# Performance work log

Measured on AMD Instinct MI355X. Metric: run time of the kernel, lower is better.

## Reference

```python
import jax, jax.numpy as jnp
import numpy as np

D_K = 64
SCALE = jnp.sqrt(jnp.float32(D_K))

def setup_inputs() -> dict:
    key = jax.random.key(0)
    kq, kk, kv = jax.random.split(key, 3)
    shape = (2, 16, 2048, D_K)  # [batch, heads, seq, d_k]
    return {
        "Q": jax.random.normal(kq, shape, dtype=jnp.float32),
        "K": jax.random.normal(kk, shape, dtype=jnp.float32),
        "V": jax.random.normal(kv, shape, dtype=jnp.float32),
    }

def reference(Q, K, V):
    # scores: [B, H, S, S]
    scores = jnp.einsum("bhqd,bhkd->bhqk", Q, K) / SCALE
    weights = jax.nn.softmax(scores, axis=-1)
    return jnp.einsum("bhqk,bhkd->bhqd", weights, V)
```

## Files before the change

kernel.cpp:

```cpp
#include <hip/hip_runtime.h>
#include <math.h>

#define S_LEN 2048
#define DK 64
#define BH 32
#define BQ 128
#define BK 64
#define NT 32
#define NTH 16
#define TILE_US 8192
#define TILE_B  16384

#if defined(__has_builtin)
#if __has_builtin(__builtin_amdgcn_exp2f)
#define EXP2F(x) __builtin_amdgcn_exp2f(x)
#else
#define EXP2F(x) exp2f(x)
#endif
#else
#define EXP2F(x) exp2f(x)
#endif

typedef _Float16 f16x8 __attribute__((ext_vector_type(8)));
typedef __fp16   fp16x2 __attribute__((ext_vector_type(2)));
typedef float    f32x16 __attribute__((ext_vector_type(16)));

#define MFMAH(a,b,c) __builtin_amdgcn_mfma_f32_32x32x16_f16((a),(b),(c),0,0,0)

union U16H { uint4 u; f16x8 h; unsigned short s[8]; };

__device__ __forceinline__ f16x8 g16(const unsigned short* p){
    U16H t; t.u = *(const uint4*)p; return t.h;
}
__device__ __forceinline__ f16x8 u4h(unsigned a, unsigned b, unsigned c, unsigned d){
    U16H t; t.u = make_uint4(a,b,c,d); return t.h;
}
__device__ __forceinline__ unsigned pk16(float a, float b){
    union { fp16x2 h; unsigned u; } c;
    c.h = __builtin_amdgcn_cvt_pkrtz(a, b);
    return c.u;
}
__device__ __forceinline__ unsigned short f16b(float x){
    union { _Float16 f; unsigned short s; } c; c.f = (_Float16)x; return c.s;
}

__global__ __launch_bounds__(256) void prep(const float* __restrict__ K,
                                            const float* __restrict__ V,
                                            unsigned short* __restrict__ W) {
    __shared__ unsigned short Vt[64 * 72];
    const int t = threadIdx.x;
    const int head = blockIdx.x >> 5;
    const int kb = blockIdx.x & 31;
    const size_t hbase = (size_t)head * S_LEN * DK;
    unsigned short* Wt = W + (size_t)(head * NT + kb) * TILE_US;

    {
        const int row = t >> 2;
        const int c0 = (t & 3) * 16;
        const float* vp = V + hbase + (size_t)(kb * BK + row) * DK + c0;
        #pragma unroll
        for (int i = 0; i < 4; ++i) {
            const float4 q = *(const float4*)(vp + 4 * i);
            const int c = c0 + 4 * i;
            Vt[(c + 0) * 72 + row] = f16b(q.x);
            Vt[(c + 1) * 72 + row] = f16b(q.y);
            Vt[(c + 2) * 72 + row] = f16b(q.z);
            Vt[(c + 3) * 72 + row] = f16b(q.w);
        }
    }
    #pragma unroll
    for (int i = 0; i < 2; ++i) {
        const int P = i * 256 + t;
        const int r = P >> 3, p = P & 7;
        const float* kp = K + hbase + (size_t)(kb * BK + r) * DK + p * 8;
        const float4 a = *(const float4*)kp;
        const float4 b = *(const float4*)(kp + 4);
        const int frag  = ((r >> 5) << 2) | (p >> 1);
        const int lane8 = ((p & 1) << 5) | (r & 31);
        *(uint4*)(Wt + frag * 512 + lane8 * 8) =
            make_uint4(pk16(a.x, a.y), pk16(a.z, a.w), pk16(b.x, b.y), pk16(b.z, b.w));
    }
    __syncthreads();
    #pragma unroll
    for (int i = 0; i < 2; ++i) {
        const int P = i * 256 + t;
        const int d = P >> 3, p = P & 7;
        const uint4 u = *(const uint4*)(Vt + d * 72 + p * 8);
        const int frag  = 8 + (((d >> 5) << 2) | (p >> 1));
        const int lane8 = ((p & 1) << 5) | (d & 31);
        *(uint4*)(Wt + frag * 512 + lane8 * 8) = u;
    }
}

__global__ __launch_bounds__(256, 2) void fa4(const float* __restrict__ Q,
                                              const unsigned short* __restrict__ W,
                                              float* __restrict__ O) {
    __shared__ __align__(16) float Mbuf[BQ * 68];
    __shared__ float Lbuf[BQ];

    const int tid = threadIdx.x;
    const int kh  = tid >> 7;
    const int wq  = (tid >> 6) & 1;
    const int lane = tid & 63;
    const int L31 = tid & 31;
    const int q5  = (tid >> 5) & 1;

    const int bid  = blockIdx.x;
    const int x    = bid & 7, g = bid >> 3;
    const int head = ((g >> 4) << 3) | x;
    const int qb   = g & 15;
    const size_t hbase = (size_t)head * S_LEN * DK;
    const unsigned short* Wh = W + (size_t)head * NT * TILE_US;

    const float c1 = 0.18033688011112042f;
    f16x8 qfA[4], qfB[4];
    {
        const int qrow = qb * BQ + wq * 64 + L31;
        const float* qpA = Q + hbase + (size_t)qrow * DK;
        const float* qpB = qpA + 32 * DK;
        #pragma unroll
        for (int ks = 0; ks < 4; ++ks) {
            float4 a = *(const float4*)(qpA + ks * 16 + q5 * 8);
            float4 b = *(const float4*)(qpA + ks * 16 + q5 * 8 + 4);
            qfA[ks] = u4h(pk16(a.x * c1, a.y * c1), pk16(a.z * c1, a.w * c1),
                          pk16(b.x * c1, b.y * c1), pk16(b.z * c1, b.w * c1));
            a = *(const float4*)(qpB + ks * 16 + q5 * 8);
            b = *(const float4*)(qpB + ks * 16 + q5 * 8 + 4);
            qfB[ks] = u4h(pk16(a.x * c1, a.y * c1), pk16(a.z * c1, a.w * c1),
                          pk16(b.x * c1, b.y * c1), pk16(b.z * c1, b.w * c1));
        }
    }

    const unsigned short* tb = Wh + (size_t)(kh * NTH) * TILE_US;
    const int lo = lane * 8;
    f16x8 ka[4], kb_[4], va[4], vb[4];
    #pragma unroll
    for (int ks = 0; ks < 4; ++ks) {
        ka[ks]  = g16(tb + ks * 512 + lo);
        kb_[ks] = g16(tb + (4 + ks) * 512 + lo);
    }
    #pragma unroll
    for (int ks = 0; ks < 4; ++ks) {
        va[ks] = g16(tb + (8 + ks) * 512 + lo);
        vb[ks] = g16(tb + (12 + ks) * 512 + lo);
    }

    f32x16 oA0 = {}, oA1 = {}, oB0 = {}, oB1 = {};
    float lA = 0.f, lB = 0.f;

    for (int it = 0; it < NTH; ++it) {
        f32x16 sA0 = {}, sA1 = {}, sB0 = {}, sB1 = {};
        #pragma unroll
        for (int ks = 0; ks < 4; ++ks) {
            sA0 = MFMAH(ka[ks],  qfA[ks], sA0);
            sA1 = MFMAH(kb_[ks], qfA[ks], sA1);
            sB0 = MFMAH(ka[ks],  qfB[ks], sB0);
            sB1 = MFMAH(kb_[ks], qfB[ks], sB1);
        }
        const unsigned short* nx = tb + TILE_US;
        #pragma unroll
        for (int ks = 0; ks < 4; ++ks) {
            ka[ks]  = g16(nx + ks * 512 + lo);
            kb_[ks] = g16(nx + (4 + ks) * 512 + lo);
        }

        float ra0 = 0.f, ra1 = 0.f, rb0 = 0.f, rb1 = 0.f;
        #pragma unroll
        for (int r = 0; r < 16; ++r) {
            sA0[r] = EXP2F(sA0[r]); ra0 += sA0[r];
            sA1[r] = EXP2F(sA1[r]); ra1 += sA1[r];
            sB0[r] = EXP2F(sB0[r]); rb0 += sB0[r];
            sB1[r] = EXP2F(sB1[r]); rb1 += sB1[r];
        }
        float rsA = ra0 + ra1;
        float rsB = rb0 + rb1;
        rsA += __shfl_xor(rsA, 32); lA += rsA;
        rsB += __shfl_xor(rsB, 32); lB += rsB;

        unsigned PA[2][4][2], PB[2][4][2];
        #pragma unroll
        for (int b = 0; b < 4; ++b) {
            PA[0][b][0] = pk16(sA0[4*b+0], sA0[4*b+1]);
            PA[0][b][1] = pk16(sA0[4*b+2], sA0[4*b+3]);
            PA[1][b][0] = pk16(sA1[4*b+0], sA1[4*b+1]);
            PA[1][b][1] = pk16(sA1[4*b+2], sA1[4*b+3]);
            PB[0][b][0] = pk16(sB0[4*b+0], sB0[4*b+1]);
            PB[0][b][1] = pk16(sB0[4*b+2], sB0[4*b+3]);
            PB[1][b][0] = pk16(sB1[4*b+0], sB1[4*b+1]);
            PB[1][b][1] = pk16(sB1[4*b+2], sB1[4*b+3]);
        }

        #pragma unroll
        for (int ks = 0; ks < 4; ++ks) {
            const int mt = ks >> 1, kk2 = (ks & 1) * 2;
            const f16x8 v0 = va[ks];
            const f16x8 v1 = vb[ks];
            {
                const unsigned own0 = q5 ? PA[mt][kk2+1][0] : PA[mt][kk2][0];
                const unsigned own1 = q5 ? PA[mt][kk2+1][1] : PA[mt][kk2][1];
                const unsigned snd0 = q5 ? PA[mt][kk2][0]   : PA[mt][kk2+1][0];
                const unsigned snd1 = q5 ? PA[mt][kk2][1]   : PA[mt][kk2+1][1];
                const unsigned r0 = (unsigned)__shfl_xor((int)snd0, 32);
                const unsigned r1 = (unsigned)__shfl_xor((int)snd1, 32);
                const f16x8 ph = q5 ? u4h(r0, r1, own0, own1) : u4h(own0, own1, r0, r1);
                oA0 = MFMAH(v0, ph, oA0);
                oA1 = MFMAH(v1, ph, oA1);
            }
            {
                const unsigned own0 = q5 ? PB[mt][kk2+1][0] : PB[mt][kk2][0];
                const unsigned own1 = q5 ? PB[mt][kk2+1][1] : PB[mt][kk2][1];
                const unsigned snd0 = q5 ? PB[mt][kk2][0]   : PB[mt][kk2+1][0];
                const unsigned snd1 = q5 ? PB[mt][kk2][1]   : PB[mt][kk2+1][1];
                const unsigned r0 = (unsigned)__shfl_xor((int)snd0, 32);
                const unsigned r1 = (unsigned)__shfl_xor((int)snd1, 32);
                const f16x8 ph = q5 ? u4h(r0, r1, own0, own1) : u4h(own0, own1, r0, r1);
                oB0 = MFMAH(v0, ph, oB0);
                oB1 = MFMAH(v1, ph, oB1);
            }
        }
        #pragma unroll
        for (int ks = 0; ks < 4; ++ks) {
            va[ks] = g16(nx + (8 + ks) * 512 + lo);
            vb[ks] = g16(nx + (12 + ks) * 512 + lo);
        }
        tb = nx;
    }

    const int qA = wq * 64 + L31;
    if (kh == 1) {
        float* mpA = Mbuf + qA * 68;
        float* mpB = mpA + 32 * 68;
        #pragma unroll
        for (int b = 0; b < 4; ++b) {
            *(float4*)(mpA + 8 * b + 4 * q5) =
                make_float4(oA0[4*b+0], oA0[4*b+1], oA0[4*b+2], oA0[4*b+3]);
            *(float4*)(mpA + 32 + 8 * b + 4 * q5) =
                make_float4(oA1[4*b+0], oA1[4*b+1], oA1[4*b+2], oA1[4*b+3]);
            *(float4*)(mpB + 8 * b + 4 * q5) =
                make_float4(oB0[4*b+0], oB0[4*b+1], oB0[4*b+2], oB0[4*b+3]);
            *(float4*)(mpB + 32 + 8 * b + 4 * q5) =
                make_float4(oB1[4*b+0], oB1[4*b+1], oB1[4*b+2], oB1[4*b+3]);
        }
        if (q5 == 0) { Lbuf[qA] = lA; Lbuf[qA + 32] = lB; }
    }
    __syncthreads();
    if (kh == 0) {
        const float invA = 1.f / (lA + Lbuf[qA]);
        const float invB = 1.f / (lB + Lbuf[qA + 32]);
        const float* mpA = Mbuf + qA * 68;
        const float* mpB = mpA + 32 * 68;
        const int qrow = qb * BQ + qA;
        float* opA = O + hbase + (size_t)qrow * DK;
        float* opB = opA + 32 * DK;
        #pragma unroll
        for (int b = 0; b < 4; ++b) {
            float4 m = *(const float4*)(mpA + 8 * b + 4 * q5);
            float4 o;
            o.x = (oA0[4*b+0] + m.x) * invA; o.y = (oA0[4*b+1] + m.y) * invA;
            o.z = (oA0[4*b+2] + m.z) * invA; o.w = (oA0[4*b+3] + m.w) * invA;
            *(float4*)(opA + 8 * b + 4 * q5) = o;
            m = *(const float4*)(mpA + 32 + 8 * b + 4 * q5);
            o.x = (oA1[4*b+0] + m.x) * invA; o.y = (oA1[4*b+1] + m.y) * invA;
            o.z = (oA1[4*b+2] + m.z) * invA; o.w = (oA1[4*b+3] + m.w) * invA;
            *(float4*)(opA + 32 + 8 * b + 4 * q5) = o;
            m = *(const float4*)(mpB + 8 * b + 4 * q5);
            o.x = (oB0[4*b+0] + m.x) * invB; o.y = (oB0[4*b+1] + m.y) * invB;
            o.z = (oB0[4*b+2] + m.z) * invB; o.w = (oB0[4*b+3] + m.w) * invB;
            *(float4*)(opB + 8 * b + 4 * q5) = o;
            m = *(const float4*)(mpB + 32 + 8 * b + 4 * q5);
            o.x = (oB1[4*b+0] + m.x) * invB; o.y = (oB1[4*b+1] + m.y) * invB;
            o.z = (oB1[4*b+2] + m.z) * invB; o.w = (oB1[4*b+3] + m.w) * invB;
            *(float4*)(opB + 32 + 8 * b + 4 * q5) = o;
        }
    }
}

extern "C" void kernel_launch(void* const* d_in, const int* in_sizes, int n_in,
                              void* d_out, int out_size, void* d_ws, size_t ws_size,
                              hipStream_t stream) {
    const float* Q = (const float*)d_in[0];
    const float* K = (const float*)d_in[1];
    const float* V = (const float*)d_in[2];
    float* O = (float*)d_out;
    unsigned short* W = (unsigned short*)d_ws;
    prep<<<dim3(BH * NT), dim3(256), 0, stream>>>(K, V, W);
    fa4<<<dim3(512), dim3(256), 0, stream>>>(Q, W, O);
}
```

Baseline: 140.9 us.

## Split keys across four waves per 64-query block with tree reduction

The attention kernel now gives each block 64 queries and splits the key sequence into four 8-tile chunks, one per wave, instead of two waves per key half over 128 queries. The partial outputs are merged with a two-stage LDS tree reduction. The grid doubles to 1024 blocks, and launch bounds move to 4 blocks per CU to raise parallelism and occupancy. MFMA sections are wrapped in s_setprio, and the prep kernel is rewritten to write coalesced fragment-ordered K/V with an fp32 LDS transpose for V. Risks are extra reduction syncs and more total Q loads.

```diff
diff --git a/kernel.cpp b/kernel.cpp
--- a/kernel.cpp
+++ b/kernel.cpp
@@ -4,10 +4,10 @@
 #define S_LEN 2048
 #define DK 64
 #define BH 32
-#define BQ 128
+#define BQ 64
 #define BK 64
 #define NT 32
-#define NTH 16
+#define NTQ 8
 #define TILE_US 8192
 #define TILE_B  16384
 
@@ -40,14 +40,11 @@
     c.h = __builtin_amdgcn_cvt_pkrtz(a, b);
     return c.u;
 }
-__device__ __forceinline__ unsigned short f16b(float x){
-    union { _Float16 f; unsigned short s; } c; c.f = (_Float16)x; return c.s;
-}
 
 __global__ __launch_bounds__(256) void prep(const float* __restrict__ K,
                                             const float* __restrict__ V,
                                             unsigned short* __restrict__ W) {
-    __shared__ unsigned short Vt[64 * 72];
+    __shared__ __align__(16) float Vs[64 * 68];
     const int t = threadIdx.x;
     const int head = blockIdx.x >> 5;
     const int kb = blockIdx.x & 31;
@@ -59,63 +56,61 @@
         const int c0 = (t & 3) * 16;
         const float* vp = V + hbase + (size_t)(kb * BK + row) * DK + c0;
         #pragma unroll
-        for (int i = 0; i < 4; ++i) {
-            const float4 q = *(const float4*)(vp + 4 * i);
-            const int c = c0 + 4 * i;
-            Vt[(c + 0) * 72 + row] = f16b(q.x);
-            Vt[(c + 1) * 72 + row] = f16b(q.y);
-            Vt[(c + 2) * 72 + row] = f16b(q.z);
-            Vt[(c + 3) * 72 + row] = f16b(q.w);
-        }
-    }
+        for (int i = 0; i < 4; ++i)
+            *(float4*)(Vs + row * 68 + c0 + 4 * i) = *(const float4*)(vp + 4 * i);
+    }
+
     #pragma unroll
     for (int i = 0; i < 2; ++i) {
         const int P = i * 256 + t;
-        const int r = P >> 3, p = P & 7;
+        const int frag = P >> 6, lane8 = P & 63;
+        const int r = ((frag >> 2) << 5) | (lane8 & 31);
+        const int p = ((frag & 3) << 1) | (lane8 >> 5);
         const float* kp = K + hbase + (size_t)(kb * BK + r) * DK + p * 8;
         const float4 a = *(const float4*)kp;
         const float4 b = *(const float4*)(kp + 4);
-        const int frag  = ((r >> 5) << 2) | (p >> 1);
-        const int lane8 = ((p & 1) << 5) | (r & 31);
-        *(uint4*)(Wt + frag * 512 + lane8 * 8) =
-            make_uint4(pk16(a.x, a.y), pk16(a.z, a.w), pk16(b.x, b.y), pk16(b.z, b.w));
+        *(uint4*)(Wt + P * 8) = make_uint4(pk16(a.x, a.y), pk16(a.z, a.w),
+                                           pk16(b.x, b.y), pk16(b.z, b.w));
     }
     __syncthreads();
+
     #pragma unroll
     for (int i = 0; i < 2; ++i) {
         const int P = i * 256 + t;
-        const int d = P >> 3, p = P & 7;
-        const uint4 u = *(const uint4*)(Vt + d * 72 + p * 8);
-        const int frag  = 8 + (((d >> 5) << 2) | (p >> 1));
-        const int lane8 = ((p & 1) << 5) | (d & 31);
-        *(uint4*)(Wt + frag * 512 + lane8 * 8) = u;
-    }
-}
-
-__global__ __launch_bounds__(256, 2) void fa4(const float* __restrict__ Q,
+        const int frag = P >> 6, lane8 = P & 63;
+        const int d  = ((frag >> 2) << 5) | (lane8 & 31);
+        const int k0 = (frag & 3) * 16 + (lane8 >> 5) * 8;
+        const float* c = Vs + k0 * 68 + d;
+        const float v0 = c[0],   v1 = c[68],  v2 = c[136], v3 = c[204];
+        const float v4 = c[272], v5 = c[340], v6 = c[408], v7 = c[476];
+        *(uint4*)(Wt + 4096 + P * 8) =
+            make_uint4(pk16(v0, v1), pk16(v2, v3), pk16(v4, v5), pk16(v6, v7));
+    }
+}
+
+__global__ __launch_bounds__(256, 4) void fa4(const float* __restrict__ Q,
                                               const unsigned short* __restrict__ W,
                                               float* __restrict__ O) {
-    __shared__ __align__(16) float Mbuf[BQ * 68];
-    __shared__ float Lbuf[BQ];
+    __shared__ __align__(16) float Mbuf[2 * 64 * 68];
+    __shared__ float Lbuf[2 * 64];
 
     const int tid = threadIdx.x;
-    const int kh  = tid >> 7;
-    const int wq  = (tid >> 6) & 1;
+    const int w    = tid >> 6;
     const int lane = tid & 63;
-    const int L31 = tid & 31;
-    const int q5  = (tid >> 5) & 1;
+    const int L31  = tid & 31;
+    const int q5   = (tid >> 5) & 1;
 
     const int bid  = blockIdx.x;
     const int x    = bid & 7, g = bid >> 3;
-    const int head = ((g >> 4) << 3) | x;
-    const int qb   = g & 15;
+    const int head = ((g >> 5) << 3) | x;
+    const int qb   = g & 31;
     const size_t hbase = (size_t)head * S_LEN * DK;
     const unsigned short* Wh = W + (size_t)head * NT * TILE_US;
 
     const float c1 = 0.18033688011112042f;
     f16x8 qfA[4], qfB[4];
     {
-        const int qrow = qb * BQ + wq * 64 + L31;
+        const int qrow = qb * BQ + L31;
         const float* qpA = Q + hbase + (size_t)qrow * DK;
         const float* qpB = qpA + 32 * DK;
         #pragma unroll
@@ -131,7 +126,7 @@
         }
     }
 
-    const unsigned short* tb = Wh + (size_t)(kh * NTH) * TILE_US;
+    const unsigned short* tb = Wh + (size_t)(w * NTQ) * TILE_US;
     const int lo = lane * 8;
     f16x8 ka[4], kb_[4], va[4], vb[4];
     #pragma unroll
@@ -148,8 +143,9 @@
     f32x16 oA0 = {}, oA1 = {}, oB0 = {}, oB1 = {};
     float lA = 0.f, lB = 0.f;
 
-    for (int it = 0; it < NTH; ++it) {
+    for (int it = 0; it < NTQ; ++it) {
         f32x16 sA0 = {}, sA1 = {}, sB0 = {}, sB1 = {};
+        __builtin_amdgcn_s_setprio(1);
         #pragma unroll
         for (int ks = 0; ks < 4; ++ks) {
             sA0 = MFMAH(ka[ks],  qfA[ks], sA0);
@@ -157,6 +153,7 @@
             sB0 = MFMAH(ka[ks],  qfB[ks], sB0);
             sB1 = MFMAH(kb_[ks], qfB[ks], sB1);
         }
+        __builtin_amdgcn_s_setprio(0);
         const unsigned short* nx = tb + TILE_US;
         #pragma unroll
         for (int ks = 0; ks < 4; ++ks) {
@@ -203,8 +200,10 @@
                 const unsigned r0 = (unsigned)__shfl_xor((int)snd0, 32);
                 const unsigned r1 = (unsigned)__shfl_xor((int)snd1, 32);
                 const f16x8 ph = q5 ? u4h(r0, r1, own0, own1) : u4h(own0, own1, r0, r1);
+                __builtin_amdgcn_s_setprio(1);
                 oA0 = MFMAH(v0, ph, oA0);
                 oA1 = MFMAH(v1, ph, oA1);
+                __builtin_amdgcn_s_setprio(0);
             }
             {
                 const unsigned own0 = q5 ? PB[mt][kk2+1][0] : PB[mt][kk2][0];
@@ -214,8 +213,10 @@
                 const unsigned r0 = (unsigned)__shfl_xor((int)snd0, 32);
                 const unsigned r1 = (unsigned)__shfl_xor((int)snd1, 32);
                 const f16x8 ph = q5 ? u4h(r0, r1, own0, own1) : u4h(own0, own1, r0, r1);
+                __builtin_amdgcn_s_setprio(1);
                 oB0 = MFMAH(v0, ph, oB0);
                 oB1 = MFMAH(v1, ph, oB1);
+                __builtin_amdgcn_s_setprio(0);
             }
         }
         #pragma unroll
@@ -226,51 +227,82 @@
         tb = nx;
     }
 
-    const int qA = wq * 64 + L31;
-    if (kh == 1) {
-        float* mpA = Mbuf + qA * 68;
-        float* mpB = mpA + 32 * 68;
-        #pragma unroll
-        for (int b = 0; b < 4; ++b) {
-            *(float4*)(mpA + 8 * b + 4 * q5) =
+    if (w >= 2) {
+        float* mp = Mbuf + (w - 2) * 4352 + L31 * 68;
+        #pragma unroll
+        for (int b = 0; b < 4; ++b) {
+            *(float4*)(mp + 8*b + 4*q5) =
                 make_float4(oA0[4*b+0], oA0[4*b+1], oA0[4*b+2], oA0[4*b+3]);
-            *(float4*)(mpA + 32 + 8 * b + 4 * q5) =
+            *(float4*)(mp + 32 + 8*b + 4*q5) =
                 make_float4(oA1[4*b+0], oA1[4*b+1], oA1[4*b+2], oA1[4*b+3]);
-            *(float4*)(mpB + 8 * b + 4 * q5) =
+            *(float4*)(mp + 32*68 + 8*b + 4*q5) =
                 make_float4(oB0[4*b+0], oB0[4*b+1], oB0[4*b+2], oB0[4*b+3]);
-            *(float4*)(mpB + 32 + 8 * b + 4 * q5) =
+            *(float4*)(mp + 32*68 + 32 + 8*b + 4*q5) =
                 make_float4(oB1[4*b+0], oB1[4*b+1], oB1[4*b+2], oB1[4*b+3]);
         }
-        if (q5 == 0) { Lbuf[qA] = lA; Lbuf[qA + 32] = lB; }
+        if (q5 == 0) { Lbuf[(w-2)*64 + L31] = lA; Lbuf[(w-2)*64 + 32 + L31] = lB; }
     }
     __syncthreads();
-    if (kh == 0) {
-        const float invA = 1.f / (lA + Lbuf[qA]);
-        const float invB = 1.f / (lB + Lbuf[qA + 32]);
-        const float* mpA = Mbuf + qA * 68;
-        const float* mpB = mpA + 32 * 68;
-        const int qrow = qb * BQ + qA;
+    if (w < 2) {
+        const float* mp = Mbuf + w * 4352 + L31 * 68;
+        #pragma unroll
+        for (int b = 0; b < 4; ++b) {
+            float4 m;
+            m = *(const float4*)(mp + 8*b + 4*q5);
+            oA0[4*b+0]+=m.x; oA0[4*b+1]+=m.y; oA0[4*b+2]+=m.z; oA0[4*b+3]+=m.w;
+            m = *(const float4*)(mp + 32 + 8*b + 4*q5);
+            oA1[4*b+0]+=m.x; oA1[4*b+1]+=m.y; oA1[4*b+2]+=m.z; oA1[4*b+3]+=m.w;
+            m = *(const float4*)(mp + 32*68 + 8*b + 4*q5);
+            oB0[4*b+0]+=m.x; oB0[4*b+1]+=m.y; oB0[4*b+2]+=m.z; oB0[4*b+3]+=m.w;
+            m = *(const float4*)(mp + 32*68 + 32 + 8*b + 4*q5);
+            oB1[4*b+0]+=m.x; oB1[4*b+1]+=m.y; oB1[4*b+2]+=m.z; oB1[4*b+3]+=m.w;
+        }
+        lA += Lbuf[w*64 + L31];
+        lB += Lbuf[w*64 + 32 + L31];
+    }
+    __syncthreads();
+    if (w == 1) {
+        float* mp = Mbuf + L31 * 68;
+        #pragma unroll
+        for (int b = 0; b < 4; ++b) {
+            *(float4*)(mp + 8*b + 4*q5) =
+                make_float4(oA0[4*b+0], oA0[4*b+1], oA0[4*b+2], oA0[4*b+3]);
+            *(float4*)(mp + 32 + 8*b + 4*q5) =
+                make_float4(oA1[4*b+0], oA1[4*b+1], oA1[4*b+2], oA1[4*b+3]);
+            *(float4*)(mp + 32*68 + 8*b + 4*q5) =
+                make_float4(oB0[4*b+0], oB0[4*b+1], oB0[4*b+2], oB0[4*b+3]);
+            *(float4*)(mp + 32*68 + 32 + 8*b + 4*q5) =
+                make_float4(oB1[4*b+0], oB1[4*b+1], oB1[4*b+2], oB1[4*b+3]);
+        }
+        if (q5 == 0) { Lbuf[L31] = lA; Lbuf[32 + L31] = lB; }
+    }
+    __syncthreads();
+    if (w == 0) {
+        const float invA = 1.f / (lA + Lbuf[L31]);
+        const float invB = 1.f / (lB + Lbuf[32 + L31]);
+        const float* mp = Mbuf + L31 * 68;
+        const int qrow = qb * BQ + L31;
         float* opA = O + hbase + (size_t)qrow * DK;
         float* opB = opA + 32 * DK;
         #pragma unroll
         for (int b = 0; b < 4; ++b) {
-            float4 m = *(const float4*)(mpA + 8 * b + 4 * q5);
+            float4 m = *(const float4*)(mp + 8*b + 4*q5);
             float4 o;
             o.x = (oA0[4*b+0] + m.x) * invA; o.y = (oA0[4*b+1] + m.y) * invA;
             o.z = (oA0[4*b+2] + m.z) * invA; o.w = (oA0[4*b+3] + m.w) * invA;
-            *(float4*)(opA + 8 * b + 4 * q5) = o;
-            m = *(const float4*)(mpA + 32 + 8 * b + 4 * q5);
+            *(float4*)(opA + 8*b + 4*q5) = o;
+            m = *(const float4*)(mp + 32 + 8*b + 4*q5);
             o.x = (oA1[4*b+0] + m.x) * invA; o.y = (oA1[4*b+1] + m.y) * invA;
             o.z = (oA1[4*b+2] + m.z) * invA; o.w = (oA1[4*b+3] + m.w) * invA;
-            *(float4*)(opA + 32 + 8 * b + 4 * q5) = o;
-            m = *(const float4*)(mpB + 8 * b + 4 * q5);
+            *(float4*)(opA + 32 + 8*b + 4*q5) = o;
+            m = *(const float4*)(mp + 32*68 + 8*b + 4*q5);
             o.x = (oB0[4*b+0] + m.x) * invB; o.y = (oB0[4*b+1] + m.y) * invB;
             o.z = (oB0[4*b+2] + m.z) * invB; o.w = (oB0[4*b+3] + m.w) * invB;
-            *(float4*)(opB + 8 * b + 4 * q5) = o;
-            m = *(const float4*)(mpB + 32 + 8 * b + 4 * q5);
+            *(float4*)(opB + 8*b + 4*q5) = o;
+            m = *(const float4*)(mp + 32*68 + 32 + 8*b + 4*q5);
             o.x = (oB1[4*b+0] + m.x) * invB; o.y = (oB1[4*b+1] + m.y) * invB;
             o.z = (oB1[4*b+2] + m.z) * invB; o.w = (oB1[4*b+3] + m.w) * invB;
-            *(float4*)(opB + 32 + 8 * b + 4 * q5) = o;
+            *(float4*)(opB + 32 + 8*b + 4*q5) = o;
         }
     }
 }
@@ -284,5 +316,5 @@
     float* O = (float*)d_out;
     unsigned short* W = (unsigned short*)d_ws;
     prep<<<dim3(BH * NT), dim3(256), 0, stream>>>(K, V, W);
-    fa4<<<dim3(512), dim3(256), 0, stream>>>(Q, W, O);
-}
+    fa4<<<dim3(BH * 32), dim3(256), 0, stream>>>(Q, W, O);
+}
```

Result: slower. 391.5 us (+177.8%).
